# Kernel optimization log

Hardware: AMD Instinct MI355X
Metric: run time of the kernel (lower is better)

The kernel has to match this reference:

```python
import jax, jax.numpy as jnp
import numpy as np
import math

T, E = 8192, 64            # tokens, experts
K_VALUE = 2                # top-2 router
CAP_FACTOR = 1.25          # capacity_factor_train (module in training mode)
MIN_CAPACITY = 4


def _get_capacity(tokens, experts):
    cap = math.floor(K_VALUE * CAP_FACTOR * tokens / experts)
    cap += cap % 2  # make even
    cap = max(cap, MIN_CAPACITY)
    assert cap > 0
    return int(cap)


def setup_inputs() -> dict:
    key = jax.random.key(0)
    inputs = jax.random.normal(key, (T, E), dtype=jnp.float32)
    return {"inputs": inputs}


def reference(inputs):
    tokens, experts = inputs.shape
    capacity = _get_capacity(tokens, experts)  # static (shape-derived)

    probs = jax.nn.softmax(inputs, axis=-1)                       # [T, E]
    top1_idx = jnp.argmax(probs, axis=-1)                         # [T]
    mask1 = jax.nn.one_hot(top1_idx, experts, dtype=jnp.int32)    # [T, E]
    probs_except1 = jnp.where(mask1.astype(bool), -jnp.inf, probs)
    top2_idx = jnp.argmax(probs_except1, axis=-1)                 # [T]
    mask2 = jax.nn.one_hot(top2_idx, experts, dtype=jnp.int32)

    # position of each token in its expert's queue (moe_cumsum = cumsum - 1)
    rank1 = jnp.cumsum(mask1, axis=0) - 1                          # [T, E]
    rank2 = jnp.cumsum(mask2, axis=0) - 1 + jnp.sum(mask1, axis=0, keepdims=True)

    # drop tokens beyond capacity
    mask1 = mask1 * (rank1 < capacity)
    mask2 = mask2 * (rank2 < capacity)
    used_capacity = mask1.sum(axis=0) + mask2.sum(axis=0)          # [E]

    # per-token slot index (0 if dropped) and gate weight (0 if dropped)
    r1 = jnp.sum(mask1 * rank1, axis=-1)                           # [T]
    r2 = jnp.sum(mask2 * rank2, axis=-1)
    w1 = jnp.sum(mask1 * probs, axis=-1)                           # [T]
    w2 = jnp.sum(mask2 * probs, axis=-1)
    m1b = jnp.sum(mask1, axis=-1).astype(bool)                     # kept flags
    m2b = jnp.sum(mask2, axis=-1).astype(bool)

    idx = jnp.arange(tokens)
    cb_weight = jnp.zeros((tokens, experts, capacity), dtype=inputs.dtype)
    cb_weight = cb_weight.at[idx, top1_idx, r1].add(w1)
    cb_weight = cb_weight.at[idx, top2_idx, r2].add(w2)

    sec_mask = jnp.zeros((tokens, experts, capacity), dtype=bool)
    sec_mask = sec_mask.at[idx, top1_idx, r1].max(m1b)
    sec_mask = sec_mask.at[idx, top2_idx, r2].max(m2b)

    return used_capacity, cb_weight, sec_mask
```

## Files before the change

### kernel.cpp

```cpp
#include <hip/hip_runtime.h>
#include <hip/hip_bf16.h>
#include <math.h>

#define T_TOKENS 8192
#define N_EXP    64
#define CAP      320

__global__ __launch_bounds__(256) void moe_topk_kernel(
    const float* __restrict__ in,
    int* __restrict__ top1, int* __restrict__ top2,
    float* __restrict__ w1, float* __restrict__ w2)
{
    const int token = blockIdx.x * 4 + (threadIdx.x >> 6);
    const int lane  = threadIdx.x & 63;
    if (token >= T_TOKENS) return;

    const float x = in[(size_t)token * N_EXP + lane];

    float v = x; int idx = lane;
    #pragma unroll
    for (int off = 32; off; off >>= 1) {
        float vo = __shfl_xor(v, off);
        int   io = __shfl_xor(idx, off);
        if (vo > v || (vo == v && io < idx)) { v = vo; idx = io; }
    }
    const float m  = v;
    const int   i1 = idx;

    float e = expf(x - m);
    float s = e;
    #pragma unroll
    for (int off = 32; off; off >>= 1) s += __shfl_xor(s, off);

    float v2 = (lane == i1) ? -INFINITY : x;
    int idx2 = lane;
    #pragma unroll
    for (int off = 32; off; off >>= 1) {
        float vo = __shfl_xor(v2, off);
        int   io = __shfl_xor(idx2, off);
        if (vo > v2 || (vo == v2 && io < idx2)) { v2 = vo; idx2 = io; }
    }

    if (lane == 0) {
        top1[token] = i1;
        top2[token] = idx2;
        w1[token]   = 1.0f / s;
        w2[token]   = expf(v2 - m) / s;
    }
}

__global__ __launch_bounds__(256) void moe_rank_scatter_kernel(
    const int* __restrict__ top1, const int* __restrict__ top2,
    const float* __restrict__ w1, const float* __restrict__ w2,
    float* __restrict__ out)
{
    const int e    = blockIdx.x;
    const int tid  = threadIdx.x;
    const int lane = tid & 63;
    const int wid  = tid >> 6;

    __shared__ int wsum[4];

    float* __restrict__ used = out;
    float* __restrict__ cb   = out + N_EXP;
    float* __restrict__ sec  = out + N_EXP + (size_t)T_TOKENS * N_EXP * CAP;

    const unsigned long long below_mask = (lane == 63)
        ? 0x7FFFFFFFFFFFFFFFull
        : ((1ull << lane) - 1ull);

    int base = 0;

    for (int t0 = 0; t0 < T_TOKENS; t0 += 256) {
        const int  t     = t0 + tid;
        const bool match = (top1[t] == e);
        const unsigned long long mb = __ballot(match);
        const int below = __popcll(mb & below_mask);
        if (lane == 0) wsum[wid] = __popcll(mb);
        __syncthreads();
        int pre = 0;
        for (int w = 0; w < wid; ++w) pre += wsum[w];
        const int tot = wsum[0] + wsum[1] + wsum[2] + wsum[3];
        if (match) {
            const int r = base + pre + below;
            if (r < CAP) {
                const size_t o = (size_t)t * N_EXP * CAP + (size_t)e * CAP + r;
                cb[o]  = w1[t];
                sec[o] = 1.0f;
            }
        }
        base += tot;
        __syncthreads();
    }
    const int count1 = base;

    int base2 = 0;
    for (int t0 = 0; t0 < T_TOKENS; t0 += 256) {
        const int  t     = t0 + tid;
        const bool match = (top2[t] == e);
        const unsigned long long mb = __ballot(match);
        const int below = __popcll(mb & below_mask);
        if (lane == 0) wsum[wid] = __popcll(mb);
        __syncthreads();
        int pre = 0;
        for (int w = 0; w < wid; ++w) pre += wsum[w];
        const int tot = wsum[0] + wsum[1] + wsum[2] + wsum[3];
        if (match) {
            const int r = count1 + base2 + pre + below;
            if (r < CAP) {
                const size_t o = (size_t)t * N_EXP * CAP + (size_t)e * CAP + r;
                cb[o]  = w2[t];
                sec[o] = 1.0f;
            }
        }
        base2 += tot;
        __syncthreads();
    }
    const int count2 = base2;

    if (tid == 0) {
        const int kept1 = min(count1, CAP);
        const int kept2 = min(max(CAP - count1, 0), count2);
        used[e] = (float)(kept1 + kept2);
    }
}

extern "C" void kernel_launch(void* const* d_in, const int* in_sizes, int n_in,
                              void* d_out, int out_size, void* d_ws, size_t ws_size,
                              hipStream_t stream) {
    const float* in  = (const float*)d_in[0];
    float*       out = (float*)d_out;

    int*   top1 = (int*)d_ws;
    int*   top2 = top1 + T_TOKENS;
    float* w1   = (float*)(top2 + T_TOKENS);
    float* w2   = w1 + T_TOKENS;

    hipMemsetAsync(d_out, 0, (size_t)out_size * sizeof(float), stream);

    moe_topk_kernel<<<T_TOKENS / 4, 256, 0, stream>>>(in, top1, top2, w1, w2);
    moe_rank_scatter_kernel<<<N_EXP, 256, 0, stream>>>(top1, top2, w1, w2, out);
}
```

Measured before the change: 268.0 us.

## Replace memset plus scattered writes with a dense per-token row-write kernel

The full-output memset and the scattered weight/mask writes are replaced by two pieces. A rank kernel now only computes each token's flat slot index, or -1 when the token is dropped. A new kernel writes every token's full cb_weight and sec_mask rows once with float4 stores, inserting the gate weights in place. This aims to avoid writing the 1.3 GB output twice and to remove the uncoalesced scatter, at the cost of an extra launch and a small index buffer in workspace.

After: 287.4 us. 1.07x slower.

```diff
diff --git a/kernel.cpp b/kernel.cpp
--- a/kernel.cpp
+++ b/kernel.cpp
@@ -5,6 +5,7 @@
 #define T_TOKENS 8192
 #define N_EXP    64
 #define CAP      320
+#define ROW4     (N_EXP * CAP / 4)
 
 __global__ __launch_bounds__(256) void moe_topk_kernel(
     const float* __restrict__ in,
@@ -27,8 +28,7 @@
     const float m  = v;
     const int   i1 = idx;
 
-    float e = expf(x - m);
-    float s = e;
+    float s = expf(x - m);
     #pragma unroll
     for (int off = 32; off; off >>= 1) s += __shfl_xor(s, off);
 
@@ -49,10 +49,10 @@
     }
 }
 
-__global__ __launch_bounds__(256) void moe_rank_scatter_kernel(
+__global__ __launch_bounds__(256) void moe_rank_kernel(
     const int* __restrict__ top1, const int* __restrict__ top2,
-    const float* __restrict__ w1, const float* __restrict__ w2,
-    float* __restrict__ out)
+    int* __restrict__ c1, int* __restrict__ c2,
+    float* __restrict__ used)
 {
     const int e    = blockIdx.x;
     const int tid  = threadIdx.x;
@@ -61,16 +61,11 @@
 
     __shared__ int wsum[4];
 
-    float* __restrict__ used = out;
-    float* __restrict__ cb   = out + N_EXP;
-    float* __restrict__ sec  = out + N_EXP + (size_t)T_TOKENS * N_EXP * CAP;
-
     const unsigned long long below_mask = (lane == 63)
         ? 0x7FFFFFFFFFFFFFFFull
         : ((1ull << lane) - 1ull);
 
     int base = 0;
-
     for (int t0 = 0; t0 < T_TOKENS; t0 += 256) {
         const int  t     = t0 + tid;
         const bool match = (top1[t] == e);
@@ -83,11 +78,7 @@
         const int tot = wsum[0] + wsum[1] + wsum[2] + wsum[3];
         if (match) {
             const int r = base + pre + below;
-            if (r < CAP) {
-                const size_t o = (size_t)t * N_EXP * CAP + (size_t)e * CAP + r;
-                cb[o]  = w1[t];
-                sec[o] = 1.0f;
-            }
+            c1[t] = (r < CAP) ? (e * CAP + r) : -1;
         }
         base += tot;
         __syncthreads();
@@ -107,11 +98,7 @@
         const int tot = wsum[0] + wsum[1] + wsum[2] + wsum[3];
         if (match) {
             const int r = count1 + base2 + pre + below;
-            if (r < CAP) {
-                const size_t o = (size_t)t * N_EXP * CAP + (size_t)e * CAP + r;
-                cb[o]  = w2[t];
-                sec[o] = 1.0f;
-            }
+            c2[t] = (r < CAP) ? (e * CAP + r) : -1;
         }
         base2 += tot;
         __syncthreads();
@@ -125,6 +112,47 @@
     }
 }
 
+__global__ __launch_bounds__(256) void moe_row_write_kernel(
+    const int* __restrict__ c1, const int* __restrict__ c2,
+    const float* __restrict__ w1, const float* __restrict__ w2,
+    float* __restrict__ out)
+{
+    const int t   = blockIdx.x;
+    const int tid = threadIdx.x;
+
+    const int   p1 = c1[t];
+    const int   p2 = c2[t];
+    const float a  = w1[t];
+    const float b  = w2[t];
+    const int   q1 = p1 >> 2;
+    const int   q2 = p2 >> 2;
+
+    float4* __restrict__ cb  = (float4*)(out + N_EXP) + (size_t)t * ROW4;
+    float4* __restrict__ sec = cb + (size_t)T_TOKENS * ROW4;
+
+    #pragma unroll
+    for (int i = 0; i < ROW4 / 256; ++i) {
+        const int idx  = i * 256 + tid;
+        const int base = idx * 4;
+        float4 v = make_float4(0.f, 0.f, 0.f, 0.f);
+        float4 s = make_float4(0.f, 0.f, 0.f, 0.f);
+        if (idx == q1 || idx == q2) {
+            float* vp = (float*)&v;
+            float* sp = (float*)&s;
+            #pragma unroll
+            for (int j = 0; j < 4; ++j) {
+                const int pos = base + j;
+                float vv = 0.f, ss = 0.f;
+                if (pos == p1) { vv += a; ss = 1.f; }
+                if (pos == p2) { vv += b; ss = 1.f; }
+                vp[j] = vv; sp[j] = ss;
+            }
+        }
+        cb[idx]  = v;
+        sec[idx] = s;
+    }
+}
+
 extern "C" void kernel_launch(void* const* d_in, const int* in_sizes, int n_in,
                               void* d_out, int out_size, void* d_ws, size_t ws_size,
                               hipStream_t stream) {
@@ -133,11 +161,12 @@
 
     int*   top1 = (int*)d_ws;
     int*   top2 = top1 + T_TOKENS;
-    float* w1   = (float*)(top2 + T_TOKENS);
+    int*   c1   = top2 + T_TOKENS;
+    int*   c2   = c1 + T_TOKENS;
+    float* w1   = (float*)(c2 + T_TOKENS);
     float* w2   = w1 + T_TOKENS;
 
-    hipMemsetAsync(d_out, 0, (size_t)out_size * sizeof(float), stream);
-
     moe_topk_kernel<<<T_TOKENS / 4, 256, 0, stream>>>(in, top1, top2, w1, w2);
-    moe_rank_scatter_kernel<<<N_EXP, 256, 0, stream>>>(top1, top2, w1, w2, out);
+    moe_rank_kernel<<<N_EXP, 256, 0, stream>>>(top1, top2, c1, c2, out);
+    moe_row_write_kernel<<<T_TOKENS, 256, 0, stream>>>(c1, c2, w1, w2, out + 0);
 }
```
